# Performance work log

Hardware: AMD Instinct MI355X
Metric: run time of the kernel (lower is better)

The kernel has to match this reference:

```python
import jax, jax.numpy as jnp
import numpy as np

# B images, N objects/image, R relations/image; D=obj/rel feature dim, H=GGNN hidden,
# NO=num object classes, NR=num relation classes, T=GGNN time steps.
B, N, R, D, H, NO, NR, T = 8, 64, 2048, 4096, 512, 151, 51, 3


def setup_inputs() -> dict:
    key = jax.random.key(0)
    ks = jax.random.split(key, 24)
    nrm = lambda k, shp: jax.random.normal(k, shp, dtype=jnp.float32) * 0.02
    im_inds = jnp.repeat(jnp.arange(B, dtype=jnp.int32), N)          # sorted per-object image ids
    img_r = jnp.repeat(jnp.arange(B, dtype=jnp.int32), R)            # per-relation image ids
    pair = jax.random.randint(ks[0], (B * R, 2), 0, N, dtype=jnp.int32) + (img_r * N)[:, None]
    rel_inds = jnp.concatenate([img_r[:, None], pair], axis=1)        # [B*R, 3]
    return dict(
        im_inds=im_inds, rel_inds=rel_inds,
        obj_fmaps=jax.random.normal(ks[1], (B * N, D), jnp.float32),
        obj_logits=jax.random.normal(ks[2], (B * N, NO), jnp.float32),
        vr=jax.random.normal(ks[3], (B * R, D), jnp.float32),
        W_obj=nrm(ks[4], (D, H)), b_obj=jnp.zeros((H,), jnp.float32),
        W_rel=nrm(ks[5], (D, H)), b_rel=jnp.zeros((H,), jnp.float32),
        W_prob=nrm(ks[6], (NO, H)), b_prob=jnp.zeros((H,), jnp.float32),
        W_so=nrm(ks[7], (H, H)), W_oo=nrm(ks[8], (H, H)),
        W_rs=nrm(ks[9], (H, H)), W_ro=nrm(ks[10], (H, H)),
        Wz=nrm(ks[11], (H, H)), Uz=nrm(ks[12], (H, H)), bz=jnp.zeros((H,), jnp.float32),
        Wr=nrm(ks[13], (H, H)), Ur=nrm(ks[14], (H, H)), br=jnp.zeros((H,), jnp.float32),
        Wh=nrm(ks[15], (H, H)), Uh=nrm(ks[16], (H, H)), bh=jnp.zeros((H,), jnp.float32),
        W_out_rel=nrm(ks[17], (2 * H, H)), b_out_rel=jnp.zeros((H,), jnp.float32),
        W_cls_rel=nrm(ks[18], (H, NR)), b_cls_rel=jnp.zeros((NR,), jnp.float32),
        W_out_obj=nrm(ks[19], (2 * H, H)), b_out_obj=jnp.zeros((H,), jnp.float32),
        W_cls_obj=nrm(ks[20], (H, NO)), b_cls_obj=jnp.zeros((NO,), jnp.float32),
    )


def reference(im_inds, rel_inds, obj_fmaps, obj_logits, vr,
              W_obj, b_obj, W_rel, b_rel, W_prob, b_prob,
              W_so, W_oo, W_rs, W_ro,
              Wz, Uz, bz, Wr, Ur, br, Wh, Uh, bh,
              W_out_rel, b_out_rel, W_cls_rel, b_cls_rel,
              W_out_obj, b_out_obj, W_cls_obj, b_cls_obj):
    # obj_probs = softmax(obj_logits); project features + class distribution into GGNN hidden
    obj_probs = jax.nn.softmax(obj_logits, axis=-1)
    xo = (obj_fmaps @ W_obj + b_obj + obj_probs @ W_prob + b_prob).reshape(B, N, H)
    xr = (vr @ W_rel + b_rel).reshape(B, R, H)
    # per-image local indices: rel_inds[rel_s:rel_e, 1:] - obj_s
    off = (jnp.arange(B, dtype=rel_inds.dtype) * N)[:, None]
    subj = rel_inds[:, 1].reshape(B, R) - off
    objn = rel_inds[:, 2].reshape(B, R) - off

    def gru(h, m):
        z = jax.nn.sigmoid(m @ Wz + h @ Uz + bz)
        r = jax.nn.sigmoid(m @ Wr + h @ Ur + br)
        hh = jnp.tanh(m @ Wh + (r * h) @ Uh + bh)
        return (1.0 - z) * h + z * hh

    def per_image(xo_i, xr_i, s, o):
        ho, hr = xo_i, xr_i
        for _ in range(T):  # fixed recurrence depth (time_step_num)
            mr = ho[s] @ W_so + ho[o] @ W_oo                               # gather obj -> rel
            mo = (jax.ops.segment_sum(hr @ W_rs, s, num_segments=N)
                  + jax.ops.segment_sum(hr @ W_ro, o, num_segments=N))     # scatter rel -> obj
            ho, hr = gru(ho, mo), gru(hr, mr)
        rel_logits = jnp.tanh(jnp.concatenate([hr, xr_i], -1) @ W_out_rel + b_out_rel) @ W_cls_rel + b_cls_rel
        obj_ref = jnp.tanh(jnp.concatenate([ho, xo_i], -1) @ W_out_obj + b_out_obj) @ W_cls_obj + b_cls_obj
        return rel_logits, obj_ref

    rel_logits, obj_ref = jax.vmap(per_image)(xo, xr, subj, objn)
    rel_logits = rel_logits.reshape(B * R, NR)
    obj_ref = obj_ref.reshape(B * N, NO)
    scpred_softmax = jax.nn.softmax(rel_logits, axis=-1)
    scent_softmax = jax.nn.softmax(obj_ref, axis=-1)
    # sgcls, inference, no obj_labels: obj_preds = argmax over classes 1..NO-1, + 1
    obj_preds = jnp.argmax(obj_ref[:, 1:], axis=-1) + 1
    return (obj_ref, obj_preds, rel_logits, scpred_softmax, scent_softmax)
```

## Files before the change

kernel.cpp:

```cpp
#include <hip/hip_runtime.h>
#include <math.h>

#define Bn   8
#define Nn   64
#define Rn   2048
#define Dn   4096
#define Hn   512
#define NOc  151
#define NRc  51
#define Tt   3
#define BNt  (Bn*Nn)
#define BRt  (Bn*Rn)
#define Mall (BRt+BNt)

typedef __attribute__((ext_vector_type(8))) short short8;
typedef __attribute__((ext_vector_type(4))) float f32x4;

__device__ __forceinline__ float sigmf(float x){ return 1.0f/(1.0f+expf(-x)); }

__device__ __forceinline__ ushort f2bf_rne(float x){
  unsigned u = __float_as_uint(x);
  unsigned r = u + 0x7FFFu + ((u>>16)&1u);
  return (ushort)(r>>16);
}
__device__ __forceinline__ float bf2f(ushort h){
  return __uint_as_float(((unsigned)h)<<16);
}

template<int BM,int BN,int ASPLIT>
__global__ __launch_bounds__(256)
void gemm_b3(const float* __restrict__ Af,
             const ushort* __restrict__ Aph, const ushort* __restrict__ Apl,
             const ushort* __restrict__ Bhg, const ushort* __restrict__ Blg,
             float* __restrict__ Cf, const float* __restrict__ Cin,
             int M,int N,int K,int lda,int ldb,int ldc,
             const float* __restrict__ bias, const float* __restrict__ bias2,
             int act,int dupoff,
             ushort* __restrict__ Cph, ushort* __restrict__ Cpl,int ldcp,int dupp,
             int swz,int mode,const int* __restrict__ rel,
             const float* __restrict__ Gso,const float* __restrict__ G1,
             int brt,float* __restrict__ Zb,
             ushort* __restrict__ RHh,ushort* __restrict__ RHl,
             float* __restrict__ Hf,
             ushort* __restrict__ HXph,ushort* __restrict__ HXpl)
{
  constexpr int MT = BM/32, NT = BN/32;
  __shared__ ushort Ah[BM*40], Al[BM*40], Bh[BN*40], Bl[BN*40];

  int bxi = blockIdx.x, byi = blockIdx.y;
  if (swz){
    int id  = byi*gridDim.x + bxi;
    int mch = gridDim.y >> 3;
    int xcd = id & 7, j = id >> 3;
    byi = xcd*mch + j % mch;
    bxi = j / mch;
  }
  const int tid  = threadIdx.x;
  const int lane = tid & 63;
  const int wid  = tid >> 6;
  const int quad = lane >> 4, l15 = lane & 15;
  const int wm = (wid>>1)*(BM/2), wn = (wid&1)*(BN/2);
  const int bm = byi*BM, bn = bxi*BN;

  constexpr int TPR = 256/BM, CPT = 32/TPR;
  const int ar = tid / TPR;
  const int ak = (tid % TPR) * CPT;
  constexpr int TPRB = 256/BN, SPT = 32/TPRB;
  const int br_ = tid / TPRB;
  const int bk  = (tid % TPRB) * SPT;
  const int grA = bm + ar;
  const int grB = bn + br_;

  f32x4 acc[MT][NT];
#pragma unroll
  for (int i=0;i<MT;i++)
#pragma unroll
    for (int j=0;j<NT;j++) acc[i][j] = (f32x4){0.f,0.f,0.f,0.f};

  float  avf[ASPLIT ? 1 : CPT];
  short8 avh[ASPLIT ? CPT/8 : 1], avl[ASPLIT ? CPT/8 : 1];
  short8 bvh[SPT/8], bvl[SPT/8];

  auto load_tile = [&](int k0){
    if constexpr (ASPLIT){
      if (grA < M){
#pragma unroll
        for (int i=0;i<CPT/8;i++){
          avh[i] = *(const short8*)(Aph + (size_t)grA*lda + k0 + ak + i*8);
          avl[i] = *(const short8*)(Apl + (size_t)grA*lda + k0 + ak + i*8);
        }
      } else {
#pragma unroll
        for (int i=0;i<CPT/8;i++){
#pragma unroll
          for (int q=0;q<8;q++){ avh[i][q]=0; avl[i][q]=0; }
        }
      }
    } else {
      if (grA < M && ((lda&3)==0) && k0 + ak + CPT <= K) {
        const float* p = Af + (size_t)grA*lda + k0 + ak;
#pragma unroll
        for (int i=0;i<CPT/4;i++) ((float4*)avf)[i] = ((const float4*)p)[i];
      } else {
#pragma unroll
        for (int i=0;i<CPT;i++){
          int gk = k0+ak+i;
          avf[i] = (grA<M && gk<K) ? Af[(size_t)grA*lda+gk] : 0.f;
        }
      }
    }
    if (grB < N){
#pragma unroll
      for (int i=0;i<SPT/8;i++){
        bvh[i] = *(const short8*)(Bhg + (size_t)grB*ldb + k0 + bk + i*8);
        bvl[i] = *(const short8*)(Blg + (size_t)grB*ldb + k0 + bk + i*8);
      }
    } else {
#pragma unroll
      for (int i=0;i<SPT/8;i++){
#pragma unroll
        for (int q=0;q<8;q++){ bvh[i][q]=0; bvl[i][q]=0; }
      }
    }
  };

  load_tile(0);

  for (int k0=0; k0<K; k0+=32) {
    if constexpr (ASPLIT){
#pragma unroll
      for (int i=0;i<CPT/8;i++){
        *(short8*)&Ah[ar*40+ak+i*8] = avh[i];
        *(short8*)&Al[ar*40+ak+i*8] = avl[i];
      }
    } else {
      ushort hs[CPT], ls[CPT];
#pragma unroll
      for (int i=0;i<CPT;i++){
        ushort h = f2bf_rne(avf[i]);
        hs[i]=h; ls[i]=f2bf_rne(avf[i]-bf2f(h));
      }
#pragma unroll
      for (int i=0;i<CPT;i+=8){
        short8 vh, vl;
#pragma unroll
        for (int q=0;q<8;q++){ vh[q]=(short)hs[i+q]; vl[q]=(short)ls[i+q]; }
        *(short8*)&Ah[ar*40+ak+i] = vh;
        *(short8*)&Al[ar*40+ak+i] = vl;
      }
    }
#pragma unroll
    for (int i=0;i<SPT/8;i++){
      *(short8*)&Bh[br_*40+bk+i*8] = bvh[i];
      *(short8*)&Bl[br_*40+bk+i*8] = bvl[i];
    }
    __syncthreads();
    if (k0+32 < K) load_tile(k0+32);
    {
      short8 afh[MT], afl[MT], bfh[NT], bfl[NT];
#pragma unroll
      for (int i=0;i<MT;i++){
        int o = (wm + i*16 + l15)*40 + quad*8;
        afh[i] = *(const short8*)&Ah[o];
        afl[i] = *(const short8*)&Al[o];
      }
#pragma unroll
      for (int j=0;j<NT;j++){
        int o = (wn + j*16 + l15)*40 + quad*8;
        bfh[j] = *(const short8*)&Bh[o];
        bfl[j] = *(const short8*)&Bl[o];
      }
#pragma unroll
      for (int i=0;i<MT;i++)
#pragma unroll
        for (int j=0;j<NT;j++)
          acc[i][j] = __builtin_amdgcn_mfma_f32_16x16x32_bf16(afh[i], bfh[j], acc[i][j], 0,0,0);
#pragma unroll
      for (int i=0;i<MT;i++)
#pragma unroll
        for (int j=0;j<NT;j++)
          acc[i][j] = __builtin_amdgcn_mfma_f32_16x16x32_bf16(afh[i], bfl[j], acc[i][j], 0,0,0);
#pragma unroll
      for (int i=0;i<MT;i++)
#pragma unroll
        for (int j=0;j<NT;j++)
          acc[i][j] = __builtin_amdgcn_mfma_f32_16x16x32_bf16(afl[i], bfh[j], acc[i][j], 0,0,0);
    }
    __syncthreads();
  }

  if (mode == 0) {
#pragma unroll
    for (int i=0;i<MT;i++){
      int gm0 = bm + wm + i*16 + quad*4;
#pragma unroll
      for (int j=0;j<NT;j++){
        int gn = bn + wn + j*16 + l15;
        if (gn >= N) continue;
#pragma unroll
        for (int r=0;r<4;r++){
          int gm = gm0 + r;
          if (gm >= M) continue;
          float v = acc[i][j][r];
          if (Cin)  v += Cin[(size_t)gm*ldc+gn];
          if (bias) v += bias[gn];
          if (act==1) v = sigmf(v);
          else if (act==2) v = tanhf(v);
          if (Cf){
            Cf[(size_t)gm*ldc+gn] = v;
            if (dupoff) Cf[(size_t)gm*ldc+gn+dupoff] = v;
          }
          if (Cph){
            ushort h_ = f2bf_rne(v);
            ushort l_ = f2bf_rne(v - bf2f(h_));
            size_t p = (size_t)gm*ldcp + gn;
            Cph[p]=h_; Cpl[p]=l_;
            if (dupp){ Cph[p+dupp]=h_; Cpl[p+dupp]=l_; }
          }
        }
      }
    }
  } else if (mode == 1) {
#pragma unroll
    for (int i=0;i<MT;i++){
#pragma unroll
      for (int r=0;r<4;r++){
        int gm = bm + wm + i*16 + quad*4 + r;
        if (gm >= M) continue;
        bool isrel = gm < brt;
        int s=0,o=0; const float* g1row = nullptr;
        if (isrel){ s = rel[gm*3+1]; o = rel[gm*3+2]; }
        else g1row = G1 + (size_t)(gm-brt)*1536;
#pragma unroll
        for (int j=0;j<NT;j++){
          int gn = bn + wn + j*16 + l15;
          float v = acc[i][j][r];
          if (gn < 512){
            float g = isrel ? Gso[(size_t)s*3072+gn] + Gso[(size_t)o*3072+1536+gn]
                            : g1row[gn];
            Zb[(size_t)gm*512+gn] = sigmf(v + g + bias[gn]);
          } else {
            int h = gn - 512;
            float g = isrel ? Gso[(size_t)s*3072+512+h] + Gso[(size_t)o*3072+2048+h]
                            : g1row[512+h];
            float rhv = sigmf(v + g + bias2[h]) * Hf[(size_t)gm*512+h];
            ushort h_ = f2bf_rne(rhv);
            ushort l_ = f2bf_rne(rhv - bf2f(h_));
            RHh[(size_t)gm*512+h]=h_; RHl[(size_t)gm*512+h]=l_;
          }
        }
      }
    }
  } else {
#pragma unroll
    for (int i=0;i<MT;i++){
#pragma unroll
      for (int r=0;r<4;r++){
        int gm = bm + wm + i*16 + quad*4 + r;
        if (gm >= M) continue;
        bool isrel = gm < brt;
        int s=0,o=0; const float* g1row = nullptr;
        if (isrel){ s = rel[gm*3+1]; o = rel[gm*3+2]; }
        else g1row = G1 + (size_t)(gm-brt)*1536;
#pragma unroll
        for (int j=0;j<NT;j++){
          int h = bn + wn + j*16 + l15;
          float v = acc[i][j][r];
          float g = isrel ? Gso[(size_t)s*3072+1024+h] + Gso[(size_t)o*3072+2560+h]
                          : g1row[1024+h];
          float hh = tanhf(v + g + bias[h]);
          size_t ix = (size_t)gm*512+h;
          float z = Zb[ix];
          float hn = (1.f-z)*Hf[ix] + z*hh;
          Hf[ix] = hn;
          ushort h_ = f2bf_rne(hn);
          ushort l_ = f2bf_rne(hn - bf2f(h_));
          size_t p = (size_t)gm*1024+h;
          HXph[p]=h_; HXpl[p]=l_;
        }
      }
    }
  }
}

__global__ __launch_bounds__(256)
void tsplit(const float* __restrict__ src,int K,int N,
            ushort* __restrict__ dh, ushort* __restrict__ dl,
            int dld,int rowoff,int koff)
{
  __shared__ float t[32][33];
  const int tx = threadIdx.x, ty = threadIdx.y;
  const int kb = blockIdx.x*32, nb = blockIdx.y*32;
#pragma unroll
  for (int r=0;r<4;r++){
    int k = kb + ty + r*8, n = nb + tx;
    t[ty+r*8][tx] = (k<K && n<N) ? src[(size_t)k*N + n] : 0.f;
  }
  __syncthreads();
#pragma unroll
  for (int r=0;r<4;r++){
    int n = nb + ty + r*8, k = kb + tx;
    if (n < N){
      float v = t[tx][ty+r*8];
      ushort h = f2bf_rne(v);
      ushort l = f2bf_rne(v - bf2f(h));
      size_t o = (size_t)(rowoff+n)*dld + koff + k;
      dh[o]=h; dl[o]=l;
    }
  }
}

__global__ __launch_bounds__(64)
void softmax_kernel(const float* __restrict__ in, float* __restrict__ out,
                    int cols, int ldi, int ldo, int padto)
{
  int row = blockIdx.x, lane = threadIdx.x;
  const float* rp = in + (size_t)row*ldi;
  float m = -INFINITY;
  for (int c = lane; c < cols; c += 64) m = fmaxf(m, rp[c]);
  for (int off = 32; off; off >>= 1) m = fmaxf(m, __shfl_xor(m, off));
  float s = 0.f;
  for (int c = lane; c < cols; c += 64) s += expf(rp[c]-m);
  for (int off = 32; off; off >>= 1) s += __shfl_xor(s, off);
  float inv = 1.f/s;
  float* op = out + (size_t)row*ldo;
  for (int c = lane; c < padto; c += 64)
    op[c] = (c < cols) ? expf(rp[c]-m)*inv : 0.f;
}

__global__ __launch_bounds__(64)
void argmax_kernel(const float* __restrict__ ref, float* __restrict__ preds)
{
  int row = blockIdx.x, lane = threadIdx.x;
  const float* rp = ref + (size_t)row*NOc;
  float bv = -INFINITY; int bi = NOc;
  for (int c = 1+lane; c < NOc; c += 64) { float v = rp[c]; if (v > bv) { bv=v; bi=c; } }
  for (int off=32; off; off>>=1) {
    float ov = __shfl_xor(bv, off); int oi = __shfl_xor(bi, off);
    if (ov > bv || (ov == bv && oi < bi)) { bv = ov; bi = oi; }
  }
  if (lane==0) preds[row] = (float)bi;
}

__global__ __launch_bounds__(64)
void segsum2(const float* __restrict__ Hf, const int* __restrict__ rel_inds,
             float* __restrict__ SumSO)
{
  __shared__ float accS[64][64];
  __shared__ float accO[64][64];
  const int t = threadIdx.x;
  const int hb = blockIdx.x*64;
  const int img = blockIdx.z;
  const int relbase = img*Rn + blockIdx.y*(Rn/4);
  for (int ob=0; ob<64; ob++){ accS[ob][t]=0.f; accO[ob][t]=0.f; }
  for (int i=0;i<Rn/4;i++){
    int r = relbase+i;
    int s = rel_inds[r*3+1] - img*64;
    int o = rel_inds[r*3+2] - img*64;
    float v = Hf[(size_t)r*512 + hb + t];
    accS[s][t]+=v; accO[o][t]+=v;
  }
  for (int ob=0;ob<64;ob++){
    size_t rowb = (size_t)(img*64+ob)*1024 + hb + t;
    atomicAdd(&SumSO[rowb],     accS[ob][t]);
    atomicAdd(&SumSO[rowb+512], accO[ob][t]);
  }
}

#define FZ0 0,nullptr,nullptr,nullptr,0,nullptr,nullptr,nullptr,nullptr,nullptr,nullptr

static void TS(hipStream_t s,const float*src,int K,int N,ushort*dh,ushort*dl,
               int dld,int rowoff,int koff,int Kpad){
  dim3 g(Kpad/32,(N+31)/32);
  tsplit<<<g,dim3(32,8),0,s>>>(src,K,N,dh,dl,dld,rowoff,koff);
}

extern "C" void kernel_launch(void* const* d_in, const int* in_sizes, int n_in,
                              void* d_out, int out_size, void* d_ws, size_t ws_size,
                              hipStream_t stream) {
  (void)in_sizes; (void)n_in; (void)out_size; (void)ws_size;
  const int*   rel_inds   = (const int*)  d_in[1];
  const float* obj_fmaps  = (const float*)d_in[2];
  const float* obj_logits = (const float*)d_in[3];
  const float* vr         = (const float*)d_in[4];
  const float* W_obj      = (const float*)d_in[5];
  const float* b_obj      = (const float*)d_in[6];
  const float* W_rel      = (const float*)d_in[7];
  const float* b_rel      = (const float*)d_in[8];
  const float* W_prob     = (const float*)d_in[9];
  const float* b_prob     = (const float*)d_in[10];
  const float* W_so       = (const float*)d_in[11];
  const float* W_oo       = (const float*)d_in[12];
  const float* W_rs       = (const float*)d_in[13];
  const float* W_ro       = (const float*)d_in[14];
  const float* Wz         = (const float*)d_in[15];
  const float* Uz         = (const float*)d_in[16];
  const float* bz         = (const float*)d_in[17];
  const float* Wr         = (const float*)d_in[18];
  const float* Ur         = (const float*)d_in[19];
  const float* br         = (const float*)d_in[20];
  const float* Wh         = (const float*)d_in[21];
  const float* Uh         = (const float*)d_in[22];
  const float* bh         = (const float*)d_in[23];
  const float* W_out_rel  = (const float*)d_in[24];
  const float* b_out_rel  = (const float*)d_in[25];
  const float* W_cls_rel  = (const float*)d_in[26];
  const float* b_cls_rel  = (const float*)d_in[27];
  const float* W_out_obj  = (const float*)d_in[28];
  const float* b_out_obj  = (const float*)d_in[29];
  const float* W_cls_obj  = (const float*)d_in[30];
  const float* b_cls_obj  = (const float*)d_in[31];

  float* out          = (float*)d_out;
  float* out_obj_ref  = out;
  float* out_preds    = out + 77312;
  float* out_rel_log  = out + 77824;
  float* out_scpred   = out + 913408;
  float* out_scent    = out + 1748992;

  char* base = (char*)d_ws; size_t off = 0;
  auto alloc = [&](size_t bytes)->void*{ void* p = base+off; off = (off+bytes+255)&~(size_t)255; return p; };
  float*  Hf    = (float*) alloc((size_t)Mall*512*4);
  ushort* HXph  = (ushort*)alloc((size_t)Mall*1024*2);
  ushort* HXpl  = (ushort*)alloc((size_t)Mall*1024*2);
  ushort* RHh   = (ushort*)alloc((size_t)Mall*512*2);
  ushort* RHl   = (ushort*)alloc((size_t)Mall*512*2);
  float*  Zb    = (float*) alloc((size_t)Mall*512*4);
  ushort* Bt3h  = (ushort*)alloc((size_t)1536*512*2);
  ushort* Bt3l  = (ushort*)alloc((size_t)1536*512*2);
  ushort* BtU2h = (ushort*)alloc((size_t)1024*512*2);
  ushort* BtU2l = (ushort*)alloc((size_t)1024*512*2);
  ushort* BtUHh = (ushort*)alloc((size_t)512*512*2);
  ushort* BtUHl = (ushort*)alloc((size_t)512*512*2);
  ushort* BtPh  = (ushort*)alloc((size_t)1536*1024*2);
  ushort* BtPl  = (ushort*)alloc((size_t)1536*1024*2);
  ushort* BtORh = (ushort*)alloc((size_t)512*1024*2);
  ushort* BtORl = (ushort*)alloc((size_t)512*1024*2);
  ushort* BtCRh = (ushort*)alloc((size_t)64*512*2);
  ushort* BtCRl = (ushort*)alloc((size_t)64*512*2);
  ushort* BtOOh = (ushort*)alloc((size_t)512*1024*2);
  ushort* BtOOl = (ushort*)alloc((size_t)512*1024*2);
  ushort* BtCOh = (ushort*)alloc((size_t)152*512*2);
  ushort* BtCOl = (ushort*)alloc((size_t)152*512*2);
  ushort* BtWCh = (ushort*)alloc((size_t)3072*512*2);
  ushort* BtWCl = (ushort*)alloc((size_t)3072*512*2);
  float*  Gso   = (float*) alloc((size_t)512*3072*4);
  float*  G1    = (float*) alloc((size_t)512*1536*4);
  float*  SumSO = (float*) alloc((size_t)512*1024*4);
  float*  oprob = (float*) alloc((size_t)512*152*4);
  float*  Xotmp = (float*) alloc((size_t)512*512*4);
  ushort* COph  = (ushort*)alloc((size_t)512*512*2);
  ushort* COpl  = (ushort*)alloc((size_t)512*512*2);

  ushort* BtRELh = (ushort*)Zb;
  ushort* BtRELl = BtRELh + (size_t)512*4096;
  ushort* BtOBJh = BtRELl + (size_t)512*4096;
  ushort* BtOBJl = BtOBJh + (size_t)512*4096;
  ushort* BtPRh  = BtOBJl + (size_t)512*4096;
  ushort* BtPRl  = BtPRh  + (size_t)512*160;
  float*  Wcat   = (float*)(BtPRl + (size_t)512*160);
  float*  Pfp    = Wcat + (size_t)512*3072;

  softmax_kernel<<<512,64,0,stream>>>(obj_logits, oprob, NOc, NOc, 152, 152);
  TS(stream, W_rel,  4096,512, BtRELh,BtRELl, 4096, 0,0, 4096);
  TS(stream, W_obj,  4096,512, BtOBJh,BtOBJl, 4096, 0,0, 4096);
  TS(stream, W_prob,  151,512, BtPRh, BtPRl,   160, 0,0,  160);
  TS(stream, Wz, 512,512, Bt3h,Bt3l, 512,    0,0, 512);
  TS(stream, Wr, 512,512, Bt3h,Bt3l, 512,  512,0, 512);
  TS(stream, Wh, 512,512, Bt3h,Bt3l, 512, 1024,0, 512);
  TS(stream, Uz, 512,512, BtU2h,BtU2l, 512,   0,0, 512);
  TS(stream, Ur, 512,512, BtU2h,BtU2l, 512, 512,0, 512);
  TS(stream, Uh, 512,512, BtUHh,BtUHl, 512, 0,0, 512);
  TS(stream, W_out_rel, 1024,512, BtORh,BtORl, 1024, 0,0, 1024);
  TS(stream, W_cls_rel,  512, 51, BtCRh,BtCRl,  512, 0,0,  512);
  TS(stream, W_out_obj, 1024,512, BtOOh,BtOOl, 1024, 0,0, 1024);
  TS(stream, W_cls_obj,  512,151, BtCOh,BtCOl,  512, 0,0,  512);

  {
    dim3 g(8,8);
    gemm_b3<64,64,0><<<g,256,0,stream>>>(obj_fmaps,nullptr,nullptr,BtOBJh,BtOBJl,
      Xotmp,nullptr, 512,512,4096, 4096,4096,512, b_obj,nullptr,0,0,
      nullptr,nullptr,0,0, 1, FZ0);
    gemm_b3<64,64,0><<<g,256,0,stream>>>(oprob,nullptr,nullptr,BtPRh,BtPRl,
      Hf+(size_t)BRt*512, Xotmp, 512,512,151, 152,160,512, b_prob,nullptr,0,0,
      HXph+(size_t)BRt*1024+512, HXpl+(size_t)BRt*1024+512, 1024, -512, 1, FZ0);
  }
  {
    dim3 g(2,256);
    gemm_b3<64,256,0><<<g,256,0,stream>>>(vr,nullptr,nullptr,BtRELh,BtRELl,
      Hf,nullptr, BRt,512,4096, 4096,4096,512, b_rel,nullptr,0,0,
      HXph+512, HXpl+512, 1024, -512, 1, FZ0);
  }
  {
    dim3 g(24,8);
    gemm_b3<64,64,0><<<g,256,0,stream>>>(W_so,nullptr,nullptr,Bt3h,Bt3l,
      Wcat,nullptr, 512,1536,512, 512,512,3072, nullptr,nullptr,0,0, nullptr,nullptr,0,0, 1, FZ0);
    gemm_b3<64,64,0><<<g,256,0,stream>>>(W_oo,nullptr,nullptr,Bt3h,Bt3l,
      Wcat+1536,nullptr, 512,1536,512, 512,512,3072, nullptr,nullptr,0,0, nullptr,nullptr,0,0, 1, FZ0);
    gemm_b3<64,64,0><<<g,256,0,stream>>>(W_rs,nullptr,nullptr,Bt3h,Bt3l,
      Pfp,nullptr, 512,1536,512, 512,512,1536, nullptr,nullptr,0,0, nullptr,nullptr,0,0, 1, FZ0);
    gemm_b3<64,64,0><<<g,256,0,stream>>>(W_ro,nullptr,nullptr,Bt3h,Bt3l,
      Pfp+(size_t)512*1536,nullptr, 512,1536,512, 512,512,1536, nullptr,nullptr,0,0, nullptr,nullptr,0,0, 1, FZ0);
  }
  TS(stream, Wcat,  512,3072, BtWCh,BtWCl,  512, 0,0,  512);
  TS(stream, Pfp,  1024,1536, BtPh, BtPl,  1024, 0,0, 1024);

  for (int t = 0; t < Tt; t++) {
    {
      dim3 g(48,8);
      gemm_b3<64,64,1><<<g,256,0,stream>>>(nullptr,HXph+(size_t)BRt*1024,HXpl+(size_t)BRt*1024,
        BtWCh,BtWCl, Gso,nullptr, 512,3072,512, 1024,512,3072,
        nullptr,nullptr,0,0, nullptr,nullptr,0,0, 1, FZ0);
    }
    hipMemsetAsync(SumSO, 0, (size_t)512*1024*4, stream);
    segsum2<<<dim3(8,4,8),64,0,stream>>>(Hf, rel_inds, SumSO);
    {
      dim3 g(24,8);
      gemm_b3<64,64,0><<<g,256,0,stream>>>(SumSO,nullptr,nullptr,BtPh,BtPl,
        G1,nullptr, 512,1536,1024, 1024,1024,1536,
        nullptr,nullptr,0,0, nullptr,nullptr,0,0, 1, FZ0);
    }
    {
      dim3 g(8,136);
      gemm_b3<128,128,1><<<g,256,0,stream>>>(nullptr,HXph,HXpl,BtU2h,BtU2l,
        nullptr,nullptr, Mall,1024,512, 1024,512,0, bz,br,0,0,
        nullptr,nullptr,0,0, 1,
        1, rel_inds, Gso, G1, BRt, Zb, RHh,RHl, Hf, nullptr,nullptr);
    }
    {
      dim3 g(4,136);
      gemm_b3<128,128,1><<<g,256,0,stream>>>(nullptr,RHh,RHl,BtUHh,BtUHl,
        nullptr,nullptr, Mall,512,512, 512,512,0, bh,nullptr,0,0,
        nullptr,nullptr,0,0, 1,
        2, rel_inds, Gso, G1, BRt, Zb, nullptr,nullptr, Hf, HXph,HXpl);
    }
  }

  {
    dim3 g(4,128);
    gemm_b3<128,128,1><<<g,256,0,stream>>>(nullptr,HXph,HXpl,BtORh,BtORl,
      nullptr,nullptr, BRt,512,1024, 1024,1024,0, b_out_rel,nullptr,2,0,
      RHh,RHl,512,0, 1, FZ0);
  }
  {
    dim3 g(1,256);
    gemm_b3<64,64,1><<<g,256,0,stream>>>(nullptr,RHh,RHl,BtCRh,BtCRl,
      out_rel_log,nullptr, BRt,NRc,512, 512,512,NRc, b_cls_rel,nullptr,0,0,
      nullptr,nullptr,0,0, 1, FZ0);
  }
  softmax_kernel<<<BRt,64,0,stream>>>(out_rel_log, out_scpred, NRc, NRc, NRc, NRc);
  {
    dim3 g(8,8);
    gemm_b3<64,64,1><<<g,256,0,stream>>>(nullptr,HXph+(size_t)BRt*1024,HXpl+(size_t)BRt*1024,
      BtOOh,BtOOl, nullptr,nullptr, 512,512,1024, 1024,1024,0, b_out_obj,nullptr,2,0,
      COph,COpl,512,0, 1, FZ0);
  }
  {
    dim3 g(3,8);
    gemm_b3<64,64,1><<<g,256,0,stream>>>(nullptr,COph,COpl,BtCOh,BtCOl,
      out_obj_ref,nullptr, 512,NOc,512, 512,512,NOc, b_cls_obj,nullptr,0,0,
      nullptr,nullptr,0,0, 1, FZ0);
  }
  softmax_kernel<<<512,64,0,stream>>>(out_obj_ref, out_scent, NOc, NOc, NOc, NOc);
  argmax_kernel<<<512,64,0,stream>>>(out_obj_ref, out_preds);
}
```

Before: 2.166 ms.

## Double-buffer GEMM tiles with async global-to-LDS B loads and XOR swizzle

The GEMM main loop now uses double-buffered shared memory. The B operand is loaded with global_load_lds straight into LDS for the next k-tile while the current tile is computed, so one barrier per iteration is dropped. The padded 40-stride layout is replaced by a 32-stride layout with an XOR swizzle to avoid bank conflicts. Because the B loads no longer bounds-check, the transposed weight buffers are padded with zero rows up to the tile width (e.g. 64 and 192 rows) through a new Npad argument. The cost is twice the LDS, which may lower occupancy, and a dependence on every B buffer being padded correctly.

```diff
diff --git a/kernel.cpp b/kernel.cpp
--- a/kernel.cpp
+++ b/kernel.cpp
@@ -25,6 +25,12 @@
 }
 __device__ __forceinline__ float bf2f(ushort h){
   return __uint_as_float(((unsigned)h)<<16);
+}
+
+__device__ __forceinline__ void async_ld16(const ushort* g, ushort* l){
+  __builtin_amdgcn_global_load_lds(
+      (const __attribute__((address_space(1))) unsigned int*)g,
+      (__attribute__((address_space(3))) unsigned int*)l, 16, 0, 0);
 }
 
 template<int BM,int BN,int ASPLIT>
@@ -45,7 +51,10 @@
              ushort* __restrict__ HXph,ushort* __restrict__ HXpl)
 {
   constexpr int MT = BM/32, NT = BN/32;
-  __shared__ ushort Ah[BM*40], Al[BM*40], Bh[BN*40], Bl[BN*40];
+  constexpr int NSEG = BN/16;
+  constexpr int SEGW = NSEG/2;
+  __shared__ ushort As[2][2][BM*32];
+  __shared__ ushort Bs[2][2][BN*32];
 
   int bxi = blockIdx.x, byi = blockIdx.y;
   if (swz){
@@ -65,11 +74,19 @@
   constexpr int TPR = 256/BM, CPT = 32/TPR;
   const int ar = tid / TPR;
   const int ak = (tid % TPR) * CPT;
-  constexpr int TPRB = 256/BN, SPT = 32/TPRB;
-  const int br_ = tid / TPRB;
-  const int bk  = (tid % TPRB) * SPT;
   const int grA = bm + ar;
-  const int grB = bn + br_;
+  const int aswz = (ar>>1)&3;
+
+  const ushort* bptr[SEGW];
+#pragma unroll
+  for (int i=0;i<SEGW;i++){
+    int seg = i*4 + wid;
+    int plane = (seg >= NSEG) ? 1 : 0;
+    int ss = seg & (NSEG-1);
+    int row = ss*16 + (lane>>2);
+    int cg = (lane&3) ^ ((row>>1)&3);
+    bptr[i] = (plane ? Blg : Bhg) + (size_t)(bn + row)*ldb + cg*8;
+  }
 
   f32x4 acc[MT][NT];
 #pragma unroll
@@ -79,9 +96,8 @@
 
   float  avf[ASPLIT ? 1 : CPT];
   short8 avh[ASPLIT ? CPT/8 : 1], avl[ASPLIT ? CPT/8 : 1];
-  short8 bvh[SPT/8], bvl[SPT/8];
-
-  auto load_tile = [&](int k0){
+
+  auto load_A = [&](int k0){
     if constexpr (ASPLIT){
       if (grA < M){
 #pragma unroll
@@ -109,29 +125,25 @@
         }
       }
     }
-    if (grB < N){
-#pragma unroll
-      for (int i=0;i<SPT/8;i++){
-        bvh[i] = *(const short8*)(Bhg + (size_t)grB*ldb + k0 + bk + i*8);
-        bvl[i] = *(const short8*)(Blg + (size_t)grB*ldb + k0 + bk + i*8);
-      }
-    } else {
-#pragma unroll
-      for (int i=0;i<SPT/8;i++){
-#pragma unroll
-        for (int q=0;q<8;q++){ bvh[i][q]=0; bvl[i][q]=0; }
-      }
-    }
   };
 
-  load_tile(0);
-
-  for (int k0=0; k0<K; k0+=32) {
+  auto issue_B = [&](int k0,int buf){
+#pragma unroll
+    for (int i=0;i<SEGW;i++){
+      int seg = i*4 + wid;
+      int plane = (seg >= NSEG) ? 1 : 0;
+      int ss = seg & (NSEG-1);
+      async_ld16(bptr[i] + k0, &Bs[buf][plane][ss*512]);
+    }
+  };
+
+  auto stage_A = [&](int buf){
     if constexpr (ASPLIT){
 #pragma unroll
       for (int i=0;i<CPT/8;i++){
-        *(short8*)&Ah[ar*40+ak+i*8] = avh[i];
-        *(short8*)&Al[ar*40+ak+i*8] = avl[i];
+        int pos = (ak/8 + i) ^ aswz;
+        *(short8*)&As[buf][0][ar*32 + pos*8] = avh[i];
+        *(short8*)&As[buf][1][ar*32 + pos*8] = avl[i];
       }
     } else {
       ushort hs[CPT], ls[CPT];
@@ -145,48 +157,63 @@
         short8 vh, vl;
 #pragma unroll
         for (int q=0;q<8;q++){ vh[q]=(short)hs[i+q]; vl[q]=(short)ls[i+q]; }
-        *(short8*)&Ah[ar*40+ak+i] = vh;
-        *(short8*)&Al[ar*40+ak+i] = vl;
-      }
-    }
-#pragma unroll
-    for (int i=0;i<SPT/8;i++){
-      *(short8*)&Bh[br_*40+bk+i*8] = bvh[i];
-      *(short8*)&Bl[br_*40+bk+i*8] = bvl[i];
+        int pos = ((ak+i)/8) ^ aswz;
+        *(short8*)&As[buf][0][ar*32 + pos*8] = vh;
+        *(short8*)&As[buf][1][ar*32 + pos*8] = vl;
+      }
+    }
+  };
+
+  auto compute = [&](int buf){
+    short8 afh[MT], afl[MT], bfh[NT], bfl[NT];
+#pragma unroll
+    for (int i=0;i<MT;i++){
+      int row = wm + i*16 + l15;
+      int o = row*32 + ((quad ^ ((row>>1)&3))*8);
+      afh[i] = *(const short8*)&As[buf][0][o];
+      afl[i] = *(const short8*)&As[buf][1][o];
+    }
+#pragma unroll
+    for (int j=0;j<NT;j++){
+      int row = wn + j*16 + l15;
+      int o = row*32 + ((quad ^ ((row>>1)&3))*8);
+      bfh[j] = *(const short8*)&Bs[buf][0][o];
+      bfl[j] = *(const short8*)&Bs[buf][1][o];
+    }
+#pragma unroll
+    for (int i=0;i<MT;i++)
+#pragma unroll
+      for (int j=0;j<NT;j++)
+        acc[i][j] = __builtin_amdgcn_mfma_f32_16x16x32_bf16(afh[i], bfh[j], acc[i][j], 0,0,0);
+#pragma unroll
+    for (int i=0;i<MT;i++)
+#pragma unroll
+      for (int j=0;j<NT;j++)
+        acc[i][j] = __builtin_amdgcn_mfma_f32_16x16x32_bf16(afh[i], bfl[j], acc[i][j], 0,0,0);
+#pragma unroll
+    for (int i=0;i<MT;i++)
+#pragma unroll
+      for (int j=0;j<NT;j++)
+        acc[i][j] = __builtin_amdgcn_mfma_f32_16x16x32_bf16(afl[i], bfh[j], acc[i][j], 0,0,0);
+  };
+
+  load_A(0);
+  issue_B(0, 0);
+  stage_A(0);
+  __syncthreads();
+
+  int cur = 0;
+  for (int k0 = 0; k0 < K; k0 += 32){
+    if (k0 + 32 < K){
+      load_A(k0+32);
+      issue_B(k0+32, cur^1);
+      compute(cur);
+      stage_A(cur^1);
+    } else {
+      compute(cur);
     }
     __syncthreads();
-    if (k0+32 < K) load_tile(k0+32);
-    {
-      short8 afh[MT], afl[MT], bfh[NT], bfl[NT];
-#pragma unroll
-      for (int i=0;i<MT;i++){
-        int o = (wm + i*16 + l15)*40 + quad*8;
-        afh[i] = *(const short8*)&Ah[o];
-        afl[i] = *(const short8*)&Al[o];
-      }
-#pragma unroll
-      for (int j=0;j<NT;j++){
-        int o = (wn + j*16 + l15)*40 + quad*8;
-        bfh[j] = *(const short8*)&Bh[o];
-        bfl[j] = *(const short8*)&Bl[o];
-      }
-#pragma unroll
-      for (int i=0;i<MT;i++)
-#pragma unroll
-        for (int j=0;j<NT;j++)
-          acc[i][j] = __builtin_amdgcn_mfma_f32_16x16x32_bf16(afh[i], bfh[j], acc[i][j], 0,0,0);
-#pragma unroll
-      for (int i=0;i<MT;i++)
-#pragma unroll
-        for (int j=0;j<NT;j++)
-          acc[i][j] = __builtin_amdgcn_mfma_f32_16x16x32_bf16(afh[i], bfl[j], acc[i][j], 0,0,0);
-#pragma unroll
-      for (int i=0;i<MT;i++)
-#pragma unroll
-        for (int j=0;j<NT;j++)
-          acc[i][j] = __builtin_amdgcn_mfma_f32_16x16x32_bf16(afl[i], bfh[j], acc[i][j], 0,0,0);
-    }
-    __syncthreads();
+    cur ^= 1;
   }
 
   if (mode == 0) {
@@ -286,7 +313,7 @@
 __global__ __launch_bounds__(256)
 void tsplit(const float* __restrict__ src,int K,int N,
             ushort* __restrict__ dh, ushort* __restrict__ dl,
-            int dld,int rowoff,int koff)
+            int dld,int rowoff,int koff,int Npad)
 {
   __shared__ float t[32][33];
   const int tx = threadIdx.x, ty = threadIdx.y;
@@ -300,7 +327,7 @@
 #pragma unroll
   for (int r=0;r<4;r++){
     int n = nb + ty + r*8, k = kb + tx;
-    if (n < N){
+    if (n < Npad){
       float v = t[tx][ty+r*8];
       ushort h = f2bf_rne(v);
       ushort l = f2bf_rne(v - bf2f(h));
@@ -370,9 +397,9 @@
 #define FZ0 0,nullptr,nullptr,nullptr,0,nullptr,nullptr,nullptr,nullptr,nullptr,nullptr
 
 static void TS(hipStream_t s,const float*src,int K,int N,ushort*dh,ushort*dl,
-               int dld,int rowoff,int koff,int Kpad){
-  dim3 g(Kpad/32,(N+31)/32);
-  tsplit<<<g,dim3(32,8),0,s>>>(src,K,N,dh,dl,dld,rowoff,koff);
+               int dld,int rowoff,int koff,int Kpad,int Npad){
+  dim3 g(Kpad/32,(Npad+31)/32);
+  tsplit<<<g,dim3(32,8),0,s>>>(src,K,N,dh,dl,dld,rowoff,koff,Npad);
 }
 
 extern "C" void kernel_launch(void* const* d_in, const int* in_sizes, int n_in,
@@ -440,8 +467,8 @@
   ushort* BtCRl = (ushort*)alloc((size_t)64*512*2);
   ushort* BtOOh = (ushort*)alloc((size_t)512*1024*2);
   ushort* BtOOl = (ushort*)alloc((size_t)512*1024*2);
-  ushort* BtCOh = (ushort*)alloc((size_t)152*512*2);
-  ushort* BtCOl = (ushort*)alloc((size_t)152*512*2);
+  ushort* BtCOh = (ushort*)alloc((size_t)192*512*2);
+  ushort* BtCOl = (ushort*)alloc((size_t)192*512*2);
   ushort* BtWCh = (ushort*)alloc((size_t)3072*512*2);
   ushort* BtWCl = (ushort*)alloc((size_t)3072*512*2);
   float*  Gso   = (float*) alloc((size_t)512*3072*4);
@@ -462,19 +489,19 @@
   float*  Pfp    = Wcat + (size_t)512*3072;
 
   softmax_kernel<<<512,64,0,stream>>>(obj_logits, oprob, NOc, NOc, 152, 152);
-  TS(stream, W_rel,  4096,512, BtRELh,BtRELl, 4096, 0,0, 4096);
-  TS(stream, W_obj,  4096,512, BtOBJh,BtOBJl, 4096, 0,0, 4096);
-  TS(stream, W_prob,  151,512, BtPRh, BtPRl,   160, 0,0,  160);
-  TS(stream, Wz, 512,512, Bt3h,Bt3l, 512,    0,0, 512);
-  TS(stream, Wr, 512,512, Bt3h,Bt3l, 512,  512,0, 512);
-  TS(stream, Wh, 512,512, Bt3h,Bt3l, 512, 1024,0, 512);
-  TS(stream, Uz, 512,512, BtU2h,BtU2l, 512,   0,0, 512);
-  TS(stream, Ur, 512,512, BtU2h,BtU2l, 512, 512,0, 512);
-  TS(stream, Uh, 512,512, BtUHh,BtUHl, 512, 0,0, 512);
-  TS(stream, W_out_rel, 1024,512, BtORh,BtORl, 1024, 0,0, 1024);
-  TS(stream, W_cls_rel,  512, 51, BtCRh,BtCRl,  512, 0,0,  512);
-  TS(stream, W_out_obj, 1024,512, BtOOh,BtOOl, 1024, 0,0, 1024);
-  TS(stream, W_cls_obj,  512,151, BtCOh,BtCOl,  512, 0,0,  512);
+  TS(stream, W_rel,  4096,512, BtRELh,BtRELl, 4096, 0,0, 4096, 512);
+  TS(stream, W_obj,  4096,512, BtOBJh,BtOBJl, 4096, 0,0, 4096, 512);
+  TS(stream, W_prob,  151,512, BtPRh, BtPRl,   160, 0,0,  160, 512);
+  TS(stream, Wz, 512,512, Bt3h,Bt3l, 512,    0,0, 512, 512);
+  TS(stream, Wr, 512,512, Bt3h,Bt3l, 512,  512,0, 512, 512);
+  TS(stream, Wh, 512,512, Bt3h,Bt3l, 512, 1024,0, 512, 512);
+  TS(stream, Uz, 512,512, BtU2h,BtU2l, 512,   0,0, 512, 512);
+  TS(stream, Ur, 512,512, BtU2h,BtU2l, 512, 512,0, 512, 512);
+  TS(stream, Uh, 512,512, BtUHh,BtUHl, 512, 0,0, 512, 512);
+  TS(stream, W_out_rel, 1024,512, BtORh,BtORl, 1024, 0,0, 1024, 512);
+  TS(stream, W_cls_rel,  512, 51, BtCRh,BtCRl,  512, 0,0,  512, 64);
+  TS(stream, W_out_obj, 1024,512, BtOOh,BtOOl, 1024, 0,0, 1024, 512);
+  TS(stream, W_cls_obj,  512,151, BtCOh,BtCOl,  512, 0,0,  512, 192);
 
   {
     dim3 g(8,8);
@@ -502,8 +529,8 @@
     gemm_b3<64,64,0><<<g,256,0,stream>>>(W_ro,nullptr,nullptr,Bt3h,Bt3l,
       Pfp+(size_t)512*1536,nullptr, 512,1536,512, 512,512,1536, nullptr,nullptr,0,0, nullptr,nullptr,0,0, 1, FZ0);
   }
-  TS(stream, Wcat,  512,3072, BtWCh,BtWCl,  512, 0,0,  512);
-  TS(stream, Pfp,  1024,1536, BtPh, BtPl,  1024, 0,0, 1024);
+  TS(stream, Wcat,  512,3072, BtWCh,BtWCl,  512, 0,0,  512, 3072);
+  TS(stream, Pfp,  1024,1536, BtPh, BtPl,  1024, 0,0, 1024, 1536);
 
   for (int t = 0; t < Tt; t++) {
     {
```

Result: slower. 2.494 ms (+15.1%).
